# Kernel optimization log

Measured on AMD Instinct MI355X. Metric: run time of the kernel, lower is better.

The kernel has to match this reference:

```python
import jax, jax.numpy as jnp
import numpy as np

N_NODES = 100000
N_HEDGES = 200000
N_INC = 1000000
N_GRAPHS = 256
H = 64        # h_dim
HE = 35       # hedge_fea_dim
HOUT = 128    # hout_dim
NL = 3        # n_layers
EPS = 1e-5


def _segment_mean(vals, idx, num_segments):
    s = jax.ops.segment_sum(vals, idx, num_segments=num_segments)
    cnt = jax.ops.segment_sum(jnp.ones((vals.shape[0],), vals.dtype), idx,
                              num_segments=num_segments)
    return s / jnp.maximum(cnt, 1.0)[:, None]


def _bn(z, g, b):
    # training-mode BatchNorm1d: batch stats, biased variance
    m = jnp.mean(z, axis=0)
    v = jnp.var(z, axis=0)
    return (z - m) * jax.lax.rsqrt(v + EPS) * g + b


def setup_inputs() -> dict:
    key = jax.random.key(0)
    ks = jax.random.split(key, 32)
    inp = {
        "x": jax.random.normal(ks[0], (N_NODES, 92), jnp.float32),
        "node_idx": jax.random.randint(ks[1], (N_INC,), 0, N_NODES),
        "hedge_idx": jax.random.randint(ks[2], (N_INC,), 0, N_HEDGES),
        "hedge_attr": jax.random.normal(ks[3], (N_HEDGES, HE), jnp.float32),
        "batch": jnp.sort(jax.random.randint(ks[4], (N_NODES,), 0, N_GRAPHS)),
    }
    s = 0.05
    cat = H + HE  # 99
    inp["embed_w"] = jax.random.normal(ks[5], (92, H), jnp.float32) * s
    inp["embed_b"] = jnp.zeros((H,), jnp.float32)
    inp["f1_w"] = jax.random.normal(ks[6], (NL, cat, HE), jnp.float32) * s
    inp["f1_b"] = jnp.zeros((NL, HE), jnp.float32)
    inp["c1_w"] = jax.random.normal(ks[7], (NL, cat, HE), jnp.float32) * s
    inp["c1_b"] = jnp.zeros((NL, HE), jnp.float32)
    inp["f2_w"] = jax.random.normal(ks[8], (NL, cat, H), jnp.float32) * s
    inp["f2_b"] = jnp.zeros((NL, H), jnp.float32)
    inp["c2_w"] = jax.random.normal(ks[9], (NL, cat, H), jnp.float32) * s
    inp["c2_b"] = jnp.zeros((NL, H), jnp.float32)
    inp["bnf_g"] = jnp.ones((NL, HE), jnp.float32)
    inp["bnf_b"] = jnp.zeros((NL, HE), jnp.float32)
    inp["bnc_g"] = jnp.ones((NL, HE), jnp.float32)
    inp["bnc_b"] = jnp.zeros((NL, HE), jnp.float32)
    inp["bno_g"] = jnp.ones((NL, H), jnp.float32)
    inp["bno_b"] = jnp.zeros((NL, H), jnp.float32)
    inp["l2_w"] = jax.random.normal(ks[10], (H, HOUT), jnp.float32) * s
    inp["l2_b"] = jnp.zeros((HOUT,), jnp.float32)
    inp["out_w"] = jax.random.normal(ks[11], (HOUT, 1), jnp.float32) * s
    inp["out_b"] = jnp.zeros((1,), jnp.float32)
    return inp


def reference(x, node_idx, hedge_idx, hedge_attr, batch,
              embed_w, embed_b, f1_w, f1_b, c1_w, c1_b,
              f2_w, f2_b, c2_w, c2_b,
              bnf_g, bnf_b, bnc_g, bnc_b, bno_g, bno_b,
              l2_w, l2_b, out_w, out_b):
    sp = jax.nn.softplus
    x = x @ embed_w + embed_b  # [N, H]
    for i in range(NL):
        # gather node feats per incidence, mean over each hyperedge
        hx = _segment_mean(x[node_idx], hedge_idx, N_HEDGES)       # [NH, H]
        msg = jnp.concatenate([hx, hedge_attr], axis=1)            # [NH, H+HE]
        z_f = _bn(msg @ f1_w[i] + f1_b[i], bnf_g[i], bnf_b[i])
        z_c = _bn(msg @ c1_w[i] + c1_b[i], bnc_g[i], bnc_b[i])
        hedge_attr = jax.nn.sigmoid(z_f) * sp(z_c)                 # [NH, HE]
        z = jnp.concatenate([x[node_idx], hedge_attr[hedge_idx]], axis=-1)  # [E, H+HE]
        o = jax.nn.sigmoid(z @ f2_w[i] + f2_b[i]) * sp(z @ c2_w[i] + c2_b[i])  # [E, H]
        o = _segment_mean(o, node_idx, N_NODES)                    # [N, H]
        o = _bn(o, bno_g[i], bno_b[i])
        x = sp(o + x)
    pooled = _segment_mean(x, batch, N_GRAPHS)                     # [G, H]
    h = sp(pooled @ l2_w + l2_b)                                   # [G, HOUT]
    return h @ out_w + out_b                                       # [G, 1]
```

## Files before the change

### kernel.cpp

```cpp
#include <hip/hip_runtime.h>
#include <math.h>

#define N_NODES 100000
#define N_HEDGES 200000
#define N_INC 1000000
#define N_GRAPHS 256
#define HD 64
#define HE 35
#define CAT 99
#define EPSB 1e-5f

typedef __attribute__((ext_vector_type(8))) short short8;
typedef __attribute__((ext_vector_type(4))) float f32x4;

__device__ __forceinline__ float sp_f(float x) {
  return fmaxf(x, 0.f) + __logf(1.f + __expf(-fabsf(x)));
}
__device__ __forceinline__ float sig_f(float x) {
  return __builtin_amdgcn_rcpf(1.f + __expf(-x));
}
__device__ __forceinline__ unsigned bfr(float x) {
  unsigned u = __float_as_uint(x);
  return (u + 0x7fffu + ((u >> 16) & 1u)) >> 16;
}
__device__ __forceinline__ unsigned pk2(float lo, float hi) {
  return bfr(lo) | (bfr(hi) << 16);
}
__device__ __forceinline__ float blo(unsigned v) { return __uint_as_float(v << 16); }
__device__ __forceinline__ float bhi(unsigned v) {
  return __uint_as_float(v & 0xffff0000u);
}
__device__ __forceinline__ float bf2f(unsigned short s) {
  return __uint_as_float(((unsigned)s) << 16);
}

__global__ __launch_bounds__(256) void k_hist(const int* __restrict__ nidx,
                                              const int* __restrict__ hidx,
                                              int* __restrict__ degN,
                                              int* __restrict__ degH,
                                              int* __restrict__ rankN,
                                              int* __restrict__ rankH) {
  int e = blockIdx.x * 256 + threadIdx.x;
  if (e >= N_INC) return;
  rankH[e] = atomicAdd(&degH[hidx[e]], 1);
  rankN[e] = atomicAdd(&degN[nidx[e]], 1);
}

#define CHB ((N_HEDGES + 255) / 256)
#define CNB ((N_NODES + 255) / 256)

__global__ __launch_bounds__(256) void k_bsum(const int* __restrict__ degH,
                                              const int* __restrict__ degN,
                                              int* __restrict__ bsum) {
  __shared__ int s[256];
  int b = blockIdx.x, t = threadIdx.x;
  const int* deg;
  int n, i;
  if (b < CHB) {
    deg = degH; n = N_HEDGES; i = b * 256 + t;
  } else {
    deg = degN; n = N_NODES; i = (b - CHB) * 256 + t;
  }
  s[t] = (i < n) ? deg[i] : 0;
  __syncthreads();
  for (int st = 128; st > 0; st >>= 1) {
    if (t < st) s[t] += s[t + st];
    __syncthreads();
  }
  if (t == 0) bsum[b] = s[0];
}

__global__ __launch_bounds__(64) void k_bscan(int* __restrict__ bsum) {
  int seg0 = (blockIdx.x == 0) ? 0 : CHB;
  int segn = (blockIdx.x == 0) ? CHB : CNB;
  int lane = threadIdx.x;
  int carry = 0;
  for (int base = 0; base < segn; base += 64) {
    int i = base + lane;
    int orig = (i < segn) ? bsum[seg0 + i] : 0;
    int v = orig;
    for (int st = 1; st < 64; st <<= 1) {
      int u = __shfl_up(v, st);
      if (lane >= st) v += u;
    }
    int total = __shfl(v, 63);
    if (i < segn) bsum[seg0 + i] = carry + (v - orig);
    carry += total;
  }
}

__global__ __launch_bounds__(256) void k_alloc2(const int* __restrict__ degH,
                                                const int* __restrict__ degN,
                                                const int* __restrict__ bsum,
                                                int* __restrict__ offH,
                                                int* __restrict__ offN,
                                                float* __restrict__ invdH,
                                                float* __restrict__ invdN) {
  __shared__ int s[256];
  int b = blockIdx.x, t = threadIdx.x;
  const int* deg;
  int* off;
  int n, i;
  bool isH = (b < CHB);
  if (isH) {
    deg = degH; off = offH; n = N_HEDGES; i = b * 256 + t;
  } else {
    deg = degN; off = offN; n = N_NODES; i = (b - CHB) * 256 + t;
  }
  int d = (i < n) ? deg[i] : 0;
  s[t] = d;
  __syncthreads();
  for (int st = 1; st < 256; st <<= 1) {
    int u = 0;
    if (t >= st) u = s[t - st];
    __syncthreads();
    if (t >= st) s[t] += u;
    __syncthreads();
  }
  if (i < n) {
    off[i] = s[t] - d + bsum[b];
    if (isH)
      invdH[i] = 1.f / (float)max(d, 1);
    else
      invdN[i] = 1.f / (float)max(d, 1);
  }
}

__global__ __launch_bounds__(256) void k_fill(const int* __restrict__ nidx,
                                              const int* __restrict__ hidx,
                                              const int* __restrict__ rankH,
                                              const int* __restrict__ rankN,
                                              const int* __restrict__ offH,
                                              const int* __restrict__ offN,
                                              int* __restrict__ permHn,
                                              int* __restrict__ permNh,
                                              int* __restrict__ offH_sent,
                                              int* __restrict__ offN_sent) {
  int e = blockIdx.x * 256 + threadIdx.x;
  if (e >= N_INC) return;
  if (e == 0) {
    *offH_sent = N_INC;
    *offN_sent = N_INC;
  }
  int nd = nidx[e], hg = hidx[e];
  permHn[offH[hg] + rankH[e]] = nd;
  permNh[offN[nd] + rankN[e]] = hg;
}

__global__ __launch_bounds__(64) void k_wpack(const float* __restrict__ f1w,
                                              const float* __restrict__ c1w,
                                              uint4* __restrict__ wpk) {
  int b = blockIdx.x;
  int layer = b / 20, rem = b % 20, ct = rem / 4, ks = rem % 4;
  int lane = threadIdx.x;
  int col = ct * 16 + (lane & 15);
  int k0 = ks * 32 + (lane >> 4) * 8;
  const float* wf = f1w + layer * CAT * HE;
  const float* wc = c1w + layer * CAT * HE;
  unsigned v[4];
#pragma unroll
  for (int p = 0; p < 4; ++p) {
    float lo = 0.f, hi = 0.f;
    int ka = k0 + p * 2, kb = ka + 1;
    if (ka < 99) {
      if (col < 35) lo = wf[ka * 35 + col];
      else if (col >= 36 && col < 71) lo = wc[ka * 35 + (col - 36)];
    }
    if (kb < 99) {
      if (col < 35) hi = wf[kb * 35 + col];
      else if (col >= 36 && col < 71) hi = wc[kb * 35 + (col - 36)];
    }
    v[p] = pk2(lo, hi);
  }
  uint4 o;
  o.x = v[0]; o.y = v[1]; o.z = v[2]; o.w = v[3];
  wpk[b * 64 + lane] = o;
}

__global__ __launch_bounds__(256) void k_cvt_ha(const float* __restrict__ src,
                                                unsigned short* __restrict__ dst,
                                                int n) {
  int t = blockIdx.x * 256 + threadIdx.x;
  if (t < n) dst[t] = (unsigned short)bfr(src[t]);
}

__global__ __launch_bounds__(256) void k_embed(const float* __restrict__ x,
                                               const float* __restrict__ w,
                                               const float* __restrict__ b,
                                               unsigned short* __restrict__ outb) {
  __shared__ float ws[92 * 64];
  __shared__ float rs[16][93];
  int tid = threadIdx.x;
  for (int i = tid; i < 92 * 64; i += 256) ws[i] = w[i];
  int r0 = blockIdx.x * 16;
  for (int i = tid; i < 16 * 92; i += 256) {
    int r = i / 92, k = i - r * 92;
    rs[r][k] = x[(r0 + r) * 92 + k];
  }
  __syncthreads();
  int h = tid & 63;
  float bias = b[h];
  for (int rr = tid >> 6; rr < 16; rr += 4) {
    float acc = bias;
    for (int k = 0; k < 92; ++k) acc += rs[rr][k] * ws[k * 64 + h];
    outb[(r0 + rr) * 64 + h] = (unsigned short)bfr(acc);
  }
}

#define GR 64
__global__ __launch_bounds__(256) void k_hedge_gemm(
    const unsigned short* __restrict__ xb, const int* __restrict__ permHn,
    const int* __restrict__ offH, const float* __restrict__ invdH,
    const unsigned short* __restrict__ hab, const uint4* __restrict__ wpk,
    unsigned short* __restrict__ z, float* __restrict__ stats) {
  __shared__ unsigned short msg[GR * 128];
  __shared__ float ps[160];
  __shared__ int bndL[4][18];
  int tid = threadIdx.x;
  int w = tid >> 6, lane = tid & 63;
  int r0 = blockIdx.x * GR;
  if (tid < 160) ps[tid] = 0.f;

  short8 bfg[5][4];
#pragma unroll
  for (int ct = 0; ct < 5; ++ct)
#pragma unroll
    for (int ks = 0; ks < 4; ++ks)
      bfg[ct][ks] = __builtin_bit_cast(short8, wpk[(ct * 4 + ks) * 64 + lane]);

  char* mb = (char*)msg;
  for (int i = tid; i < GR * 64; i += 256) {
    int r = i >> 6, c = 64 + (i & 63);
    unsigned short hv = 0;
    if (c < 99) hv = hab[(size_t)(r0 + r) * 35 + (c - 64)];
    *(unsigned short*)(mb + ((r * 256 + c * 2) ^ ((r & 7) << 4))) = hv;
  }

  int r0w = r0 + w * 16;
  if (lane < 17) bndL[w][lane] = offH[r0w + lane];
  int eBeg = bndL[w][0], eEnd = bndL[w][16];

  int j = 0;
  int nb = bndL[w][1];
  float acc = 0.f;
  for (int chunk = eBeg; chunk < eEnd; chunk += 16) {
    float v[16];
#pragma unroll
    for (int t = 0; t < 16; ++t) {
      int idx = permHn[min(chunk + t, eEnd - 1)];
      v[t] = bf2f(xb[(size_t)idx * 64 + lane]);
    }
#pragma unroll
    for (int t = 0; t < 16; ++t) {
      int e = chunk + t;
      if (e >= eEnd) break;
      while (e >= nb) {
        int rl = w * 16 + j;
        unsigned short mv = (unsigned short)bfr(acc * invdH[r0w + j]);
        *(unsigned short*)(mb + ((rl * 256 + lane * 2) ^ ((rl & 7) << 4))) = mv;
        acc = 0.f;
        ++j;
        nb = bndL[w][j + 1];
      }
      acc += v[t];
    }
  }
  for (; j < 16; ++j) {
    int rl = w * 16 + j;
    unsigned short mv = (unsigned short)bfr(acc * invdH[r0w + j]);
    *(unsigned short*)(mb + ((rl * 256 + lane * 2) ^ ((rl & 7) << 4))) = mv;
    acc = 0.f;
  }
  __syncthreads();

  {
    int rloc = w * 16 + (lane & 15);
    short8 a[4];
#pragma unroll
    for (int ks = 0; ks < 4; ++ks) {
      int byte = rloc * 256 + (ks * 32 + (lane >> 4) * 8) * 2;
      a[ks] = *(const short8*)(mb + (byte ^ ((rloc & 7) << 4)));
    }
#pragma unroll
    for (int ct = 0; ct < 5; ++ct) {
      f32x4 acc4 = {0.f, 0.f, 0.f, 0.f};
#pragma unroll
      for (int ks = 0; ks < 4; ++ks)
        acc4 = __builtin_amdgcn_mfma_f32_16x16x32_bf16(a[ks], bfg[ct][ks], acc4, 0, 0, 0);
      float s = (acc4[0] + acc4[1]) + (acc4[2] + acc4[3]);
      float q = (acc4[0] * acc4[0] + acc4[1] * acc4[1]) +
                (acc4[2] * acc4[2] + acc4[3] * acc4[3]);
      s += __shfl_xor(s, 16);
      s += __shfl_xor(s, 32);
      q += __shfl_xor(q, 16);
      q += __shfl_xor(q, 32);
      int col = ct * 16 + (lane & 15);
      if ((lane >> 4) == 0 && col < 72) {
        atomicAdd(&ps[col], s);
        atomicAdd(&ps[80 + col], q);
      }
      int growb = r0 + w * 16 + ((lane >> 4) << 2);
      if (col < 72) {
#pragma unroll
        for (int r = 0; r < 4; ++r)
          z[(size_t)(growb + r) * 72 + col] = (unsigned short)bfr(acc4[r]);
      }
    }
  }
  __syncthreads();
  if (tid < 160) atomicAdd(&stats[tid], ps[tid]);
}

__global__ __launch_bounds__(256) void k_hedge_post(
    const unsigned short* __restrict__ z, const float* __restrict__ stats,
    const float* __restrict__ gf, const float* __restrict__ bf_,
    const float* __restrict__ gc, const float* __restrict__ bc_,
    const float* __restrict__ f2wb, const float* __restrict__ c2wb,
    const float* __restrict__ f2b, const float* __restrict__ c2b,
    unsigned short* __restrict__ hab, unsigned* __restrict__ Vfc) {
  __shared__ float wf[35 * 64];
  __shared__ float wc[35 * 64];
  __shared__ float rs[16][36];
  __shared__ float sf[4][35];
  int tid = threadIdx.x;
  for (int i = tid; i < 35 * 64; i += 256) {
    wf[i] = f2wb[i];
    wc[i] = c2wb[i];
  }
  if (tid < 35) {
    const float inv = 1.f / N_HEDGES;
    float mf = stats[tid] * inv;
    float vf = stats[80 + tid] * inv - mf * mf;
    float mc = stats[36 + tid] * inv;
    float vc = stats[116 + tid] * inv - mc * mc;
    float a = rsqrtf(vf + EPSB) * gf[tid];
    float b = rsqrtf(vc + EPSB) * gc[tid];
    sf[0][tid] = a;
    sf[1][tid] = bf_[tid] - mf * a;
    sf[2][tid] = b;
    sf[3][tid] = bc_[tid] - mc * b;
  }
  __syncthreads();
  int r0 = blockIdx.x * 16;
  for (int i = tid; i < 16 * 35; i += 256) {
    int r = i / 35, c = i - r * 35;
    const unsigned short* zr = &z[(size_t)(r0 + r) * 72];
    float nf = bf2f(zr[c]) * sf[0][c] + sf[1][c];
    float nc = bf2f(zr[36 + c]) * sf[2][c] + sf[3][c];
    float ha = sig_f(nf) * sp_f(nc);
    rs[r][c] = ha;
    hab[(size_t)(r0 + r) * 35 + c] = (unsigned short)bfr(ha);
  }
  __syncthreads();
  int h = tid & 63, rb = tid >> 6;
  float af0, af1, af2, af3, ac0, ac1, ac2, ac3;
  af0 = af1 = af2 = af3 = f2b[h];
  ac0 = ac1 = ac2 = ac3 = c2b[h];
  for (int k = 0; k < 35; ++k) {
    float wfv = wf[k * 64 + h], wcv = wc[k * 64 + h];
    float m0 = rs[rb][k], m1 = rs[rb + 4][k], m2 = rs[rb + 8][k], m3 = rs[rb + 12][k];
    af0 += m0 * wfv; ac0 += m0 * wcv;
    af1 += m1 * wfv; ac1 += m1 * wcv;
    af2 += m2 * wfv; ac2 += m2 * wcv;
    af3 += m3 * wfv; ac3 += m3 * wcv;
  }
  int row = r0 + rb;
  Vfc[row * 64 + h] = pk2(af0, ac0);
  Vfc[(row + 4) * 64 + h] = pk2(af1, ac1);
  Vfc[(row + 8) * 64 + h] = pk2(af2, ac2);
  Vfc[(row + 12) * 64 + h] = pk2(af3, ac3);
}

__global__ __launch_bounds__(256) void k_uv_node(const unsigned short* __restrict__ xb,
                                                 const float* __restrict__ f2w,
                                                 const float* __restrict__ c2w,
                                                 unsigned* __restrict__ Ufc) {
  __shared__ float wf[64 * 64];
  __shared__ float wc[64 * 64];
  __shared__ float rs[16][65];
  int tid = threadIdx.x;
  for (int i = tid; i < 64 * 64; i += 256) {
    wf[i] = f2w[i];
    wc[i] = c2w[i];
  }
  int r0 = blockIdx.x * 16;
  for (int i = tid; i < 16 * 64; i += 256) {
    int r = i >> 6, k = i & 63;
    rs[r][k] = bf2f(xb[(size_t)(r0 + r) * 64 + k]);
  }
  __syncthreads();
  int h = tid & 63, rb = tid >> 6;
  float af0 = 0, af1 = 0, af2 = 0, af3 = 0, ac0 = 0, ac1 = 0, ac2 = 0, ac3 = 0;
  for (int k = 0; k < 64; ++k) {
    float wfv = wf[k * 64 + h], wcv = wc[k * 64 + h];
    float m0 = rs[rb][k], m1 = rs[rb + 4][k], m2 = rs[rb + 8][k], m3 = rs[rb + 12][k];
    af0 += m0 * wfv; ac0 += m0 * wcv;
    af1 += m1 * wfv; ac1 += m1 * wcv;
    af2 += m2 * wfv; ac2 += m2 * wcv;
    af3 += m3 * wfv; ac3 += m3 * wcv;
  }
  int row = r0 + rb;
  Ufc[row * 64 + h] = pk2(af0, ac0);
  Ufc[(row + 4) * 64 + h] = pk2(af1, ac1);
  Ufc[(row + 8) * 64 + h] = pk2(af2, ac2);
  Ufc[(row + 12) * 64 + h] = pk2(af3, ac3);
}

__device__ __forceinline__ float act2(float uf, float uc, unsigned v) {
  float a = uf + blo(v);
  float b = uc + bhi(v);
  return sig_f(a) * sp_f(b);
}
__global__ __launch_bounds__(256) void k_node_aggr(const int* __restrict__ permNh,
                                                   const int* __restrict__ offN,
                                                   const float* __restrict__ invdN,
                                                   const unsigned* __restrict__ Ufc,
                                                   const unsigned* __restrict__ Vfc,
                                                   unsigned short* __restrict__ ob,
                                                   float* __restrict__ stats) {
  __shared__ int bndL[4][18];
  __shared__ float ls[2][4][64];
  int tid = threadIdx.x;
  int w = tid >> 6, lane = tid & 63;
  int r0w = blockIdx.x * 64 + w * 16;
  if (lane < 17) bndL[w][lane] = offN[min(r0w + lane, N_NODES)];
  int eBeg = bndL[w][0], eEnd = bndL[w][16];

  int j = 0;
  int nb = bndL[w][1];
  float acc = 0.f, sacc = 0.f, qacc = 0.f;
  unsigned u0 = (r0w < N_NODES) ? Ufc[(size_t)r0w * 64 + lane] : 0u;
  float uf = blo(u0), uc = bhi(u0);

  for (int chunk = eBeg; chunk < eEnd; chunk += 16) {
    unsigned pv[16];
#pragma unroll
    for (int t = 0; t < 16; ++t) {
      int hg = permNh[min(chunk + t, eEnd - 1)];
      pv[t] = Vfc[(size_t)hg * 64 + lane];
    }
#pragma unroll
    for (int t = 0; t < 16; ++t) {
      int e = chunk + t;
      if (e >= eEnd) break;
      while (e >= nb) {
        int row = r0w + j;
        float val = acc * invdN[row];
        ob[(size_t)row * 64 + lane] = (unsigned short)bfr(val);
        sacc += val;
        qacc += val * val;
        acc = 0.f;
        ++j;
        nb = bndL[w][j + 1];
        unsigned un = Ufc[(size_t)(r0w + j) * 64 + lane];
        uf = blo(un);
        uc = bhi(un);
      }
      acc += act2(uf, uc, pv[t]);
    }
  }
  for (; j < 16; ++j) {
    int row = r0w + j;
    if (row < N_NODES) {
      float val = acc * invdN[row];
      ob[(size_t)row * 64 + lane] = (unsigned short)bfr(val);
      sacc += val;
      qacc += val * val;
    }
    acc = 0.f;
  }

  ls[0][w][lane] = sacc;
  ls[1][w][lane] = qacc;
  __syncthreads();
  if (tid < 64) {
    atomicAdd(&stats[lane],
              ls[0][0][lane] + ls[0][1][lane] + ls[0][2][lane] + ls[0][3][lane]);
  } else if (tid < 128) {
    int hh = tid - 64;
    atomicAdd(&stats[64 + hh],
              ls[1][0][hh] + ls[1][1][hh] + ls[1][2][hh] + ls[1][3][hh]);
  }
}

__global__ __launch_bounds__(256) void k_update(unsigned short* __restrict__ xb,
                                                const unsigned short* __restrict__ ob,
                                                const float* __restrict__ stats,
                                                const float* __restrict__ g,
                                                const float* __restrict__ b) {
  int t = blockIdx.x * 256 + threadIdx.x;
  int h = t & 63;
  float mean = stats[h] * (1.f / N_NODES);
  float var = stats[64 + h] * (1.f / N_NODES) - mean * mean;
  float is = rsqrtf(var + EPSB);
  float v = (bf2f(ob[t]) - mean) * is * g[h] + b[h];
  float r = sp_f(v + bf2f(xb[t]));
  xb[t] = (unsigned short)bfr(r);
}

#define PR 512
__global__ __launch_bounds__(256) void k_pool(const unsigned short* __restrict__ xb,
                                              const int* __restrict__ batch,
                                              float* __restrict__ pooled,
                                              float* __restrict__ gcnt) {
  int h = threadIdx.x & 63, rs = threadIdx.x >> 6;
  int r0 = blockIdx.x * PR;
  int rend = min(r0 + PR, N_NODES);
  int gcur = -1;
  float acc = 0.f;
  int cnt = 0;
  for (int r = r0 + rs; r < rend; r += 4) {
    int g = batch[r];
    if (g != gcur) {
      if (gcur >= 0) {
        atomicAdd(&pooled[gcur * 64 + h], acc);
        if (h == 0) atomicAdd(&gcnt[gcur], (float)cnt);
      }
      gcur = g;
      acc = 0.f;
      cnt = 0;
    }
    acc += bf2f(xb[(size_t)r * 64 + h]);
    cnt++;
  }
  if (gcur >= 0) {
    atomicAdd(&pooled[gcur * 64 + h], acc);
    if (h == 0) atomicAdd(&gcnt[gcur], (float)cnt);
  }
}

__global__ __launch_bounds__(128) void k_final(const float* __restrict__ pooled,
                                               const float* __restrict__ gcnt,
                                               const float* __restrict__ l2w,
                                               const float* __restrict__ l2b,
                                               const float* __restrict__ ow,
                                               const float* __restrict__ ob,
                                               float* __restrict__ out) {
  int g = blockIdx.x;
  int t = threadIdx.x;
  __shared__ float row[64];
  __shared__ float hh[128];
  if (t < 64) row[t] = pooled[g * 64 + t] / fmaxf(gcnt[g], 1.f);
  __syncthreads();
  float acc = l2b[t];
  for (int k = 0; k < 64; ++k) acc += row[k] * l2w[k * 128 + t];
  hh[t] = sp_f(acc) * ow[t];
  __syncthreads();
  for (int s = 64; s > 0; s >>= 1) {
    if (t < s) hh[t] += hh[t + s];
    __syncthreads();
  }
  if (t == 0) out[g] = hh[0] + ob[0];
}

extern "C" void kernel_launch(void* const* d_in, const int* in_sizes, int n_in,
                              void* d_out, int out_size, void* d_ws, size_t ws_size,
                              hipStream_t stream) {
  const float* x_in = (const float*)d_in[0];
  const int* node_idx = (const int*)d_in[1];
  const int* hedge_idx = (const int*)d_in[2];
  const float* hedge_attr = (const float*)d_in[3];
  const int* batch = (const int*)d_in[4];
  const float* embed_w = (const float*)d_in[5];
  const float* embed_b = (const float*)d_in[6];
  const float* f1_w = (const float*)d_in[7];
  const float* c1_w = (const float*)d_in[9];
  const float* f2_w = (const float*)d_in[11];
  const float* f2_b = (const float*)d_in[12];
  const float* c2_w = (const float*)d_in[13];
  const float* c2_b = (const float*)d_in[14];
  const float* bnf_g = (const float*)d_in[15];
  const float* bnf_b = (const float*)d_in[16];
  const float* bnc_g = (const float*)d_in[17];
  const float* bnc_b = (const float*)d_in[18];
  const float* bno_g = (const float*)d_in[19];
  const float* bno_b = (const float*)d_in[20];
  const float* l2_w = (const float*)d_in[21];
  const float* l2_b = (const float*)d_in[22];
  const float* out_w = (const float*)d_in[23];
  const float* out_b = (const float*)d_in[24];

  char* base = (char*)d_ws;
  size_t off = 0;
  auto alloc = [&](size_t bytes) {
    size_t o = off;
    off = (off + bytes + 255) & ~(size_t)255;
    return o;
  };
  unsigned short* xbf = (unsigned short*)(base + alloc((size_t)N_NODES * 64 * 2));
  unsigned short* hab = (unsigned short*)(base + alloc((size_t)N_HEDGES * 35 * 2));
  unsigned* Vfc = (unsigned*)(base + alloc((size_t)N_HEDGES * 64 * 4));
  unsigned short* zbuf = (unsigned short*)(base + alloc((size_t)N_HEDGES * 72 * 2));
  unsigned short* obuf = (unsigned short*)(base + alloc((size_t)N_NODES * 64 * 2));
  unsigned* Ufc = (unsigned*)(base + alloc((size_t)N_NODES * 64 * 4));
  uint4* wpk = (uint4*)(base + alloc((size_t)60 * 64 * 16));
  float* hstatsA = (float*)(base + alloc(3 * 160 * 4));
  float* ostatsA = (float*)(base + alloc(3 * 128 * 4));
  float* pooled = (float*)(base + alloc((size_t)N_GRAPHS * 64 * 4));
  float* gcnt = (float*)(base + alloc((size_t)N_GRAPHS * 4));
  int* degH = (int*)(base + alloc((size_t)N_HEDGES * 4));
  int* degN = (int*)(base + alloc((size_t)N_NODES * 4));
  int* offH = (int*)(base + alloc((size_t)(N_HEDGES + 1) * 4));
  int* offN = (int*)(base + alloc((size_t)(N_NODES + 1) * 4));
  float* invdH = (float*)(base + alloc((size_t)N_HEDGES * 4));
  float* invdN = (float*)(base + alloc((size_t)N_NODES * 4));
  int* bsum = (int*)(base + alloc((size_t)(CHB + CNB) * 4));
  int* rankH = (int*)(base + alloc((size_t)N_INC * 4));
  int* rankN = (int*)(base + alloc((size_t)N_INC * 4));
  int* permHn = (int*)(base + alloc((size_t)N_INC * 4));
  int* permNh = (int*)(base + alloc((size_t)N_INC * 4));
  (void)ws_size;
  (void)in_sizes;
  (void)n_in;
  (void)out_size;

  hipMemsetAsync(degH, 0,
                 (size_t)((char*)degN - (char*)degH) + (size_t)N_NODES * 4, stream);
  k_hist<<<(N_INC + 255) / 256, 256, 0, stream>>>(node_idx, hedge_idx, degN, degH,
                                                  rankN, rankH);
  k_bsum<<<CHB + CNB, 256, 0, stream>>>(degH, degN, bsum);
  k_bscan<<<2, 64, 0, stream>>>(bsum);
  k_alloc2<<<CHB + CNB, 256, 0, stream>>>(degH, degN, bsum, offH, offN, invdH, invdN);
  k_fill<<<(N_INC + 255) / 256, 256, 0, stream>>>(node_idx, hedge_idx, rankH, rankN,
                                                  offH, offN, permHn, permNh,
                                                  &offH[N_HEDGES], &offN[N_NODES]);
  k_wpack<<<60, 64, 0, stream>>>(f1_w, c1_w, wpk);
  k_cvt_ha<<<(N_HEDGES * 35 + 255) / 256, 256, 0, stream>>>(hedge_attr, hab,
                                                            N_HEDGES * 35);
  k_embed<<<N_NODES / 16, 256, 0, stream>>>(x_in, embed_w, embed_b, xbf);

  hipMemsetAsync(hstatsA, 0, (size_t)((char*)ostatsA - (char*)hstatsA) + 3 * 128 * 4,
                 stream);

  for (int i = 0; i < 3; ++i) {
    float* hstats = hstatsA + i * 160;
    float* ostats = ostatsA + i * 128;

    k_hedge_gemm<<<N_HEDGES / GR, 256, 0, stream>>>(
        xbf, permHn, offH, invdH, hab, wpk + (size_t)i * 20 * 64, zbuf, hstats);
    k_hedge_post<<<N_HEDGES / 16, 256, 0, stream>>>(
        zbuf, hstats, bnf_g + i * HE, bnf_b + i * HE, bnc_g + i * HE, bnc_b + i * HE,
        f2_w + i * CAT * 64 + 64 * 64, c2_w + i * CAT * 64 + 64 * 64,
        f2_b + i * 64, c2_b + i * 64, hab, Vfc);

    k_uv_node<<<N_NODES / 16, 256, 0, stream>>>(xbf, f2_w + i * CAT * 64,
                                                c2_w + i * CAT * 64, Ufc);

    k_node_aggr<<<(N_NODES + 63) / 64, 256, 0, stream>>>(permNh, offN, invdN, Ufc,
                                                         Vfc, obuf, ostats);

    k_update<<<N_NODES * 64 / 256, 256, 0, stream>>>(xbf, obuf, ostats,
                                                     bno_g + i * 64, bno_b + i * 64);
  }

  hipMemsetAsync(pooled, 0, (size_t)((char*)gcnt - (char*)pooled) + N_GRAPHS * 4,
                 stream);
  k_pool<<<(N_NODES + PR - 1) / PR, 256, 0, stream>>>(xbf, batch, pooled, gcnt);
  k_final<<<N_GRAPHS, 128, 0, stream>>>(pooled, gcnt, l2_w, l2_b, out_w, out_b,
                                        (float*)d_out);
}
```

Baseline: 1.234 ms.

## Fuse BN update with next-layer node projection and drop hedge-attr conversion pass

The residual BatchNorm/softplus update is fused with the next layer's node-side U projection, so the updated fp32 row stays in shared memory instead of being re-read as bf16 by a separate kernel. The first layer's hedge GEMM converts fp32 hedge_attr to bf16 on the fly, which removes the standalone conversion kernel. The last layer skips writing the hedge attributes, since nothing reads them afterwards. This saves a few launches and global round trips. The U projection now uses fp32 x values rather than bf16-rounded ones, which slightly changes numerics.

```diff
diff --git a/kernel.cpp b/kernel.cpp
--- a/kernel.cpp
+++ b/kernel.cpp
@@ -177,13 +177,6 @@
   wpk[b * 64 + lane] = o;
 }
 
-__global__ __launch_bounds__(256) void k_cvt_ha(const float* __restrict__ src,
-                                                unsigned short* __restrict__ dst,
-                                                int n) {
-  int t = blockIdx.x * 256 + threadIdx.x;
-  if (t < n) dst[t] = (unsigned short)bfr(src[t]);
-}
-
 __global__ __launch_bounds__(256) void k_embed(const float* __restrict__ x,
                                                const float* __restrict__ w,
                                                const float* __restrict__ b,
@@ -208,11 +201,13 @@
 }
 
 #define GR 64
+template <bool L0>
 __global__ __launch_bounds__(256) void k_hedge_gemm(
     const unsigned short* __restrict__ xb, const int* __restrict__ permHn,
     const int* __restrict__ offH, const float* __restrict__ invdH,
-    const unsigned short* __restrict__ hab, const uint4* __restrict__ wpk,
-    unsigned short* __restrict__ z, float* __restrict__ stats) {
+    const unsigned short* __restrict__ hab, const float* __restrict__ haf,
+    const uint4* __restrict__ wpk, unsigned short* __restrict__ z,
+    float* __restrict__ stats) {
   __shared__ unsigned short msg[GR * 128];
   __shared__ float ps[160];
   __shared__ int bndL[4][18];
@@ -232,7 +227,12 @@
   for (int i = tid; i < GR * 64; i += 256) {
     int r = i >> 6, c = 64 + (i & 63);
     unsigned short hv = 0;
-    if (c < 99) hv = hab[(size_t)(r0 + r) * 35 + (c - 64)];
+    if (c < 99) {
+      if (L0)
+        hv = (unsigned short)bfr(haf[(size_t)(r0 + r) * 35 + (c - 64)]);
+      else
+        hv = hab[(size_t)(r0 + r) * 35 + (c - 64)];
+    }
     *(unsigned short*)(mb + ((r * 256 + c * 2) ^ ((r & 7) << 4))) = hv;
   }
 
@@ -317,7 +317,7 @@
     const float* __restrict__ gc, const float* __restrict__ bc_,
     const float* __restrict__ f2wb, const float* __restrict__ c2wb,
     const float* __restrict__ f2b, const float* __restrict__ c2b,
-    unsigned short* __restrict__ hab, unsigned* __restrict__ Vfc) {
+    unsigned short* __restrict__ hab, unsigned* __restrict__ Vfc, int writeHa) {
   __shared__ float wf[35 * 64];
   __shared__ float wc[35 * 64];
   __shared__ float rs[16][36];
@@ -349,7 +349,7 @@
     float nc = bf2f(zr[36 + c]) * sf[2][c] + sf[3][c];
     float ha = sig_f(nf) * sp_f(nc);
     rs[r][c] = ha;
-    hab[(size_t)(r0 + r) * 35 + c] = (unsigned short)bfr(ha);
+    if (writeHa) hab[(size_t)(r0 + r) * 35 + c] = (unsigned short)bfr(ha);
   }
   __syncthreads();
   int h = tid & 63, rb = tid >> 6;
@@ -481,6 +481,50 @@
     atomicAdd(&stats[64 + hh],
               ls[1][0][hh] + ls[1][1][hh] + ls[1][2][hh] + ls[1][3][hh]);
   }
+}
+
+__global__ __launch_bounds__(256) void k_update_uv(
+    unsigned short* __restrict__ xb, const unsigned short* __restrict__ ob,
+    const float* __restrict__ stats, const float* __restrict__ g,
+    const float* __restrict__ b, const float* __restrict__ f2w,
+    const float* __restrict__ c2w, unsigned* __restrict__ Ufc) {
+  __shared__ float wf[64 * 64];
+  __shared__ float wc[64 * 64];
+  __shared__ float rs[16][65];
+  int tid = threadIdx.x;
+  for (int i = tid; i < 64 * 64; i += 256) {
+    wf[i] = f2w[i];
+    wc[i] = c2w[i];
+  }
+  int r0 = blockIdx.x * 16;
+  int h = tid & 63, rb = tid >> 6;
+  float mean = stats[h] * (1.f / N_NODES);
+  float var = stats[64 + h] * (1.f / N_NODES) - mean * mean;
+  float is = rsqrtf(var + EPSB);
+  float gh = g[h], bh = b[h];
+#pragma unroll
+  for (int j = 0; j < 16; j += 4) {
+    size_t t = (size_t)(r0 + rb + j) * 64 + h;
+    float v = (bf2f(ob[t]) - mean) * is * gh + bh;
+    float r = sp_f(v + bf2f(xb[t]));
+    xb[t] = (unsigned short)bfr(r);
+    rs[rb + j][h] = r;
+  }
+  __syncthreads();
+  float af0 = 0, af1 = 0, af2 = 0, af3 = 0, ac0 = 0, ac1 = 0, ac2 = 0, ac3 = 0;
+  for (int k = 0; k < 64; ++k) {
+    float wfv = wf[k * 64 + h], wcv = wc[k * 64 + h];
+    float m0 = rs[rb][k], m1 = rs[rb + 4][k], m2 = rs[rb + 8][k], m3 = rs[rb + 12][k];
+    af0 += m0 * wfv; ac0 += m0 * wcv;
+    af1 += m1 * wfv; ac1 += m1 * wcv;
+    af2 += m2 * wfv; ac2 += m2 * wcv;
+    af3 += m3 * wfv; ac3 += m3 * wcv;
+  }
+  int row = r0 + rb;
+  Ufc[row * 64 + h] = pk2(af0, ac0);
+  Ufc[(row + 4) * 64 + h] = pk2(af1, ac1);
+  Ufc[(row + 8) * 64 + h] = pk2(af2, ac2);
+  Ufc[(row + 12) * 64 + h] = pk2(af3, ac3);
 }
 
 __global__ __launch_bounds__(256) void k_update(unsigned short* __restrict__ xb,
@@ -625,32 +669,40 @@
                                                   offH, offN, permHn, permNh,
                                                   &offH[N_HEDGES], &offN[N_NODES]);
   k_wpack<<<60, 64, 0, stream>>>(f1_w, c1_w, wpk);
-  k_cvt_ha<<<(N_HEDGES * 35 + 255) / 256, 256, 0, stream>>>(hedge_attr, hab,
-                                                            N_HEDGES * 35);
   k_embed<<<N_NODES / 16, 256, 0, stream>>>(x_in, embed_w, embed_b, xbf);
 
   hipMemsetAsync(hstatsA, 0, (size_t)((char*)ostatsA - (char*)hstatsA) + 3 * 128 * 4,
                  stream);
+
+  k_uv_node<<<N_NODES / 16, 256, 0, stream>>>(xbf, f2_w, c2_w, Ufc);
 
   for (int i = 0; i < 3; ++i) {
     float* hstats = hstatsA + i * 160;
     float* ostats = ostatsA + i * 128;
 
-    k_hedge_gemm<<<N_HEDGES / GR, 256, 0, stream>>>(
-        xbf, permHn, offH, invdH, hab, wpk + (size_t)i * 20 * 64, zbuf, hstats);
+    if (i == 0)
+      k_hedge_gemm<true><<<N_HEDGES / GR, 256, 0, stream>>>(
+          xbf, permHn, offH, invdH, hab, hedge_attr, wpk, zbuf, hstats);
+    else
+      k_hedge_gemm<false><<<N_HEDGES / GR, 256, 0, stream>>>(
+          xbf, permHn, offH, invdH, hab, hedge_attr, wpk + (size_t)i * 20 * 64, zbuf,
+          hstats);
     k_hedge_post<<<N_HEDGES / 16, 256, 0, stream>>>(
         zbuf, hstats, bnf_g + i * HE, bnf_b + i * HE, bnc_g + i * HE, bnc_b + i * HE,
         f2_w + i * CAT * 64 + 64 * 64, c2_w + i * CAT * 64 + 64 * 64,
-        f2_b + i * 64, c2_b + i * 64, hab, Vfc);
-
-    k_uv_node<<<N_NODES / 16, 256, 0, stream>>>(xbf, f2_w + i * CAT * 64,
-                                                c2_w + i * CAT * 64, Ufc);
+        f2_b + i * 64, c2_b + i * 64, hab, Vfc, (i < 2) ? 1 : 0);
 
     k_node_aggr<<<(N_NODES + 63) / 64, 256, 0, stream>>>(permNh, offN, invdN, Ufc,
                                                          Vfc, obuf, ostats);
 
-    k_update<<<N_NODES * 64 / 256, 256, 0, stream>>>(xbf, obuf, ostats,
-                                                     bno_g + i * 64, bno_b + i * 64);
+    if (i < 2)
+      k_update_uv<<<N_NODES / 16, 256, 0, stream>>>(
+          xbf, obuf, ostats, bno_g + i * 64, bno_b + i * 64,
+          f2_w + (i + 1) * CAT * 64, c2_w + (i + 1) * CAT * 64, Ufc);
+    else
+      k_update<<<N_NODES * 64 / 256, 256, 0, stream>>>(xbf, obuf, ostats,
+                                                       bno_g + i * 64,
+                                                       bno_b + i * 64);
   }
 
   hipMemsetAsync(pooled, 0, (size_t)((char*)gcnt - (char*)pooled) + N_GRAPHS * 4,
```

After: 1.203 ms. 2.5% less time.
